# Kernel optimization log

Hardware: AMD Instinct MI355X
Metric: run time of the kernel (lower is better)

The kernel has to match this reference:

```python
import jax, jax.numpy as jnp
import numpy as np

IN_F, OUT_F, GROUP = 4096, 11008, 128
N_GROUPS = IN_F // GROUP  # 32 (in_features divisible by group_size -> no padding)


def setup_inputs() -> dict:
    key = jax.random.key(0)
    kx, kw, ks, kb = jax.random.split(key, 4)
    x = jax.random.normal(kx, (4, 2048, IN_F), dtype=jnp.float32)
    weight_q = jax.random.randint(kw, (OUT_F, IN_F), -128, 128, dtype=jnp.int32).astype(jnp.int8)
    scales = jax.random.uniform(ks, (OUT_F, N_GROUPS), dtype=jnp.float32) * 0.01 + 1e-4
    bias = jax.random.normal(kb, (OUT_F,), dtype=jnp.float32)
    return {"x": x, "weight_q": weight_q, "scales": scales, "bias": bias}


def reference(x, weight_q, scales, bias):
    # Dequantize: group-wise scale along in_features, cast to fp16 (as torch .half())
    W = (weight_q.astype(jnp.float32).reshape(OUT_F, N_GROUPS, GROUP)
         * scales[:, :, None]).reshape(OUT_F, IN_F).astype(jnp.float16)
    # fp16 linear: y = x W^T + b, then back to fp32
    y = jnp.einsum('bsi,oi->bso', x.astype(jnp.float16), W) + bias.astype(jnp.float16)
    return y.astype(jnp.float32)
```

## Files before the change

### kernel.cpp

```cpp
#include <hip/hip_runtime.h>

#define IN_F 4096
#define OUT_F 11008
#define NGROUPS 32
#define M_TOTAL 8192
#define BM 256
#define BN 256
#define BK 64
#define NKT (IN_F / BK)

typedef _Float16 half_t;
typedef __attribute__((ext_vector_type(8))) _Float16 half8;
typedef __attribute__((ext_vector_type(4))) _Float16 half4v;
typedef __attribute__((ext_vector_type(4))) float f32x4;
typedef __attribute__((ext_vector_type(4))) int i32x4;

typedef __attribute__((address_space(1))) const void gvoid_t;
typedef __attribute__((address_space(3))) void lvoid_t;

__global__ void convert_x_k(const float* __restrict__ x, half_t* __restrict__ xh) {
  const int n4 = M_TOTAL * IN_F / 4;
  int stride = gridDim.x * blockDim.x;
  for (int i = blockIdx.x * blockDim.x + threadIdx.x; i < n4; i += stride) {
    f32x4 v = __builtin_nontemporal_load((const f32x4*)x + i);
    half4v h;
    h[0] = (_Float16)v[0]; h[1] = (_Float16)v[1];
    h[2] = (_Float16)v[2]; h[3] = (_Float16)v[3];
    ((half4v*)xh)[i] = h;
  }
}

__global__ void dequant_w_k(const int* __restrict__ wq,
                            const float* __restrict__ scales,
                            half_t* __restrict__ wh) {
  int row = blockIdx.x;
  int t = threadIdx.x;
  size_t base = (size_t)row * IN_F + (size_t)t * 8;
  float s = scales[row * NGROUPS + (t >> 4)];
  i32x4 q0 = __builtin_nontemporal_load((const i32x4*)(wq + base));
  i32x4 q1 = __builtin_nontemporal_load((const i32x4*)(wq + base) + 1);
  half8 h;
#pragma unroll
  for (int j = 0; j < 4; ++j) h[j] = (_Float16)((float)q0[j] * s);
#pragma unroll
  for (int j = 0; j < 4; ++j) h[4 + j] = (_Float16)((float)q1[j] * s);
  *(half8*)(wh + base) = h;
}


__device__ __forceinline__ void rd4(half8 (&d)[4], const char* base) {
#pragma unroll
  for (int i = 0; i < 4; ++i) d[i] = *(const half8*)(base + i * 1024);
}

__device__ __forceinline__ void mfma16(f32x4 (&acc)[8][4], const half8 (&a)[4],
                                       const half8 (&b)[4], int mh) {
#pragma unroll
  for (int i = 0; i < 4; ++i)
#pragma unroll
    for (int j = 0; j < 4; ++j)
      acc[mh * 4 + i][j] =
          __builtin_amdgcn_mfma_f32_16x16x32_f16(a[i], b[j], acc[mh * 4 + i][j], 0, 0, 0);
}

#define BAR() __builtin_amdgcn_s_barrier()
#define SB0() __builtin_amdgcn_sched_barrier(0)
#define PRIO1() __builtin_amdgcn_s_setprio(1)
#define PRIO0() __builtin_amdgcn_s_setprio(0)
#define VMCNT(N) asm volatile("s_waitcnt vmcnt(" #N ")" ::: "memory")
#define LGKM(N) asm volatile("s_waitcnt lgkmcnt(" #N ")" ::: "memory")

#define STAGE(OP, KH, KT, S)                                                          \
  do {                                                                                \
    const half_t* g_ = ((OP) ? pBsrc : pAsrc) + (KT) * 64 + (KH) * 32;                \
    char* d_ = (char*)&lds[S][OP][KH][0] + wvoff;                                     \
    __builtin_amdgcn_global_load_lds((gvoid_t*)g_, (lvoid_t*)d_, 16, 0, 0);           \
    __builtin_amdgcn_global_load_lds((gvoid_t*)(g_ + 128 * IN_F),                     \
                                     (lvoid_t*)(d_ + 8192), 16, 0, 0);                \
  } while (0)

#define MPH(SL, KH, S1OP, S1KT, S1SL, S1KH, S2OP, S2KT, S2SL, S2KH, FENCE)   \
  do {                                                                       \
    rd4(a0, (const char*)&lds[SL][0][KH][0] + aoff);                         \
    rd4(a1, (const char*)&lds[SL][0][KH][0] + aoff + 4096);                  \
    rd4(b, (const char*)&lds[SL][1][KH][0] + boff);                          \
    STAGE(S1OP, S1KH, S1KT, S1SL);                                           \
    STAGE(S2OP, S2KH, S2KT, S2SL);                                           \
    SB0(); BAR();                                                            \
    LGKM(0); SB0(); PRIO1();                                                 \
    mfma16(acc, a0, b, 0);                                                   \
    mfma16(acc, a1, b, 1);                                                   \
    PRIO0();                                                                 \
    if ((FENCE) == 8) VMCNT(8);                                              \
    BAR(); SB0();                                                            \
  } while (0)

#define MPHN(SL, KH, FENCE)                                                  \
  do {                                                                       \
    rd4(a0, (const char*)&lds[SL][0][KH][0] + aoff);                         \
    rd4(a1, (const char*)&lds[SL][0][KH][0] + aoff + 4096);                  \
    rd4(b, (const char*)&lds[SL][1][KH][0] + boff);                          \
    SB0(); BAR();                                                            \
    LGKM(0); SB0(); PRIO1();                                                 \
    mfma16(acc, a0, b, 0);                                                   \
    mfma16(acc, a1, b, 1);                                                   \
    PRIO0();                                                                 \
    if ((FENCE) == 4) VMCNT(4);                                              \
    if ((FENCE) == 0) VMCNT(0);                                              \
    BAR(); SB0();                                                            \
  } while (0)

__global__ __launch_bounds__(512, 1) void gemm_k(const half_t* __restrict__ A,
                                                 const half_t* __restrict__ B,
                                                 const float* __restrict__ bias,
                                                 float* __restrict__ C) {
  __shared__ __align__(16) half_t lds[2][2][2][8192];

  const int tid = threadIdx.x;
  const int lane = tid & 63;
  const int wv = tid >> 6;
  const int wm = wv >> 2;
  const int wn = wv & 3;
  const int wvoff = wv << 10;

  const int nwg = gridDim.x;
  const int perx = nwg >> 3;
  const int L = ((int)blockIdx.x & 7) * perx + ((int)blockIdx.x >> 3);
  const int band = L >> 7;
  const int rr_ = L & 127;
  const int bn0 = band << 2;
  const int cols = (43 - bn0) < 4 ? (43 - bn0) : 4;
  const int bm = rr_ / cols;
  const int bn = bn0 + rr_ % cols;
  const int row0 = bm * BM;
  const int col0 = bn * BN;

  const int c16 = (tid & 3) * 16;
  const int srow = tid >> 2;
  const int clog = c16 ^ ((srow & 6) << 3);
  const int kidx = clog >> 1;
  const half_t* pAsrc = A + (size_t)(row0 + srow) * IN_F + kidx;
  const half_t* pBsrc = B + (size_t)(col0 + srow) * IN_F + kidx;

  const int r16 = lane & 15;
  const int kg = lane >> 4;
  const int arow = wm * 128 + r16;
  const int brow = wn * 64 + r16;
  const int aoff = arow * 64 + ((kg * 16) ^ ((arow & 6) << 3));
  const int boff = brow * 64 + ((kg * 16) ^ ((brow & 6) << 3));

  f32x4 acc[8][4];
#pragma unroll
  for (int m = 0; m < 8; ++m)
#pragma unroll
    for (int n = 0; n < 4; ++n) acc[m][n] = (f32x4){0.f, 0.f, 0.f, 0.f};

  STAGE(0, 0, 0, 0);
  STAGE(1, 0, 0, 0);
  STAGE(0, 1, 0, 0);
  STAGE(1, 1, 0, 0);
  STAGE(0, 0, 1, 1);
  STAGE(1, 0, 1, 1);
  VMCNT(4);
  BAR();
  SB0();

  half8 a0[4], a1[4], b[4];
  for (int u = 0; u < 31; ++u) {
    const int t1 = 2 * u + 1, n0 = 2 * u + 2, n1 = 2 * u + 3;
    MPH(0, 0, 0, t1, 1, 1, 1, t1, 1, 1, 8);
    MPH(0, 1, 0, n0, 0, 0, 1, n0, 0, 0, 8);
    MPH(1, 0, 0, n0, 0, 1, 1, n0, 0, 1, 8);
    MPH(1, 1, 0, n1, 1, 0, 1, n1, 1, 0, 8);
  }
  {
    MPH(0, 0, 0, 63, 1, 1, 1, 63, 1, 1, 8);
    MPHN(0, 1, 4);
    MPHN(1, 0, 0);
    MPHN(1, 1, -1);
  }

  const int kg4 = kg * 4;
#pragma unroll
  for (int nf = 0; nf < 4; ++nf) {
    int col = col0 + wn * 64 + nf * 16 + r16;
    _Float16 bh = (_Float16)bias[col];
#pragma unroll
    for (int mf = 0; mf < 8; ++mf) {
      int rb = row0 + wm * 128 + mf * 16 + kg4;
#pragma unroll
      for (int r = 0; r < 4; ++r) {
        _Float16 v = (_Float16)acc[mf][nf][r] + bh;
        __builtin_nontemporal_store((float)v, &C[(size_t)(rb + r) * OUT_F + col]);
      }
    }
  }
}

__global__ void naive_k(const float* __restrict__ x, const int* __restrict__ wq,
                        const float* __restrict__ scales, const float* __restrict__ bias,
                        float* __restrict__ out) {
  long idx = (long)blockIdx.x * blockDim.x + threadIdx.x;
  if (idx >= (long)M_TOTAL * OUT_F) return;
  int m = (int)(idx / OUT_F);
  int n = (int)(idx % OUT_F);
  float acc = 0.f;
  for (int g = 0; g < NGROUPS; ++g) {
    float s = scales[n * NGROUPS + g];
    for (int k = g * 128; k < (g + 1) * 128; ++k) {
      _Float16 xv = (_Float16)x[(size_t)m * IN_F + k];
      _Float16 wv = (_Float16)((float)wq[(size_t)n * IN_F + k] * s);
      acc += (float)xv * (float)wv;
    }
  }
  _Float16 r = (_Float16)acc + (_Float16)bias[n];
  out[idx] = (float)r;
}

extern "C" void kernel_launch(void* const* d_in, const int* in_sizes, int n_in,
                              void* d_out, int out_size, void* d_ws, size_t ws_size,
                              hipStream_t stream) {
  const float* x = (const float*)d_in[0];
  const int* wq = (const int*)d_in[1];
  const float* scales = (const float*)d_in[2];
  const float* bias = (const float*)d_in[3];
  float* out = (float*)d_out;

  const size_t xh_bytes = (size_t)M_TOTAL * IN_F * sizeof(half_t);
  const size_t wh_bytes = (size_t)OUT_F * IN_F * sizeof(half_t);

  if (ws_size >= xh_bytes + wh_bytes) {
    half_t* xh = (half_t*)d_ws;
    half_t* wh = (half_t*)((char*)d_ws + xh_bytes);
    convert_x_k<<<2048, 256, 0, stream>>>(x, xh);
    dequant_w_k<<<OUT_F, 512, 0, stream>>>(wq, scales, wh);
    gemm_k<<<(M_TOTAL / BM) * (OUT_F / BN), 512, 0, stream>>>(xh, wh, bias, out);
  } else {
    long total = (long)M_TOTAL * OUT_F;
    naive_k<<<(int)((total + 255) / 256), 256, 0, stream>>>(x, wq, scales, bias, out);
  }
}
```

Before: 786.8 us.

## Shrink GEMM tile to 256x128x32 with triple-buffered LDS and higher occupancy

Replaces the 256x256x64 tile, which used a double-buffered half-K pipeline at one block per CU, with a 256x128 tile and BK=32. LDS becomes three stages, prefetching two K-tiles ahead. Launch bounds now allow four blocks per CU, and the grid swizzle becomes a simple column-band mapping. Each wave holds a 64x64 accumulator instead of 128x64. The aim is more resident waves to hide latency, but each tile reuses its operands less, synchronises more often per FLOP, and needs a different grid size on the host.

```diff
diff --git a/kernel.cpp b/kernel.cpp
--- a/kernel.cpp
+++ b/kernel.cpp
@@ -5,8 +5,8 @@
 #define NGROUPS 32
 #define M_TOTAL 8192
 #define BM 256
-#define BN 256
-#define BK 64
+#define BN 128
+#define BK 32
 #define NKT (IN_F / BK)
 
 typedef _Float16 half_t;
@@ -48,21 +48,6 @@
 }
 
 
-__device__ __forceinline__ void rd4(half8 (&d)[4], const char* base) {
-#pragma unroll
-  for (int i = 0; i < 4; ++i) d[i] = *(const half8*)(base + i * 1024);
-}
-
-__device__ __forceinline__ void mfma16(f32x4 (&acc)[8][4], const half8 (&a)[4],
-                                       const half8 (&b)[4], int mh) {
-#pragma unroll
-  for (int i = 0; i < 4; ++i)
-#pragma unroll
-    for (int j = 0; j < 4; ++j)
-      acc[mh * 4 + i][j] =
-          __builtin_amdgcn_mfma_f32_16x16x32_f16(a[i], b[j], acc[mh * 4 + i][j], 0, 0, 0);
-}
-
 #define BAR() __builtin_amdgcn_s_barrier()
 #define SB0() __builtin_amdgcn_sched_barrier(0)
 #define PRIO1() __builtin_amdgcn_s_setprio(1)
@@ -70,70 +55,58 @@
 #define VMCNT(N) asm volatile("s_waitcnt vmcnt(" #N ")" ::: "memory")
 #define LGKM(N) asm volatile("s_waitcnt lgkmcnt(" #N ")" ::: "memory")
 
-#define STAGE(OP, KH, KT, S)                                                          \
-  do {                                                                                \
-    const half_t* g_ = ((OP) ? pBsrc : pAsrc) + (KT) * 64 + (KH) * 32;                \
-    char* d_ = (char*)&lds[S][OP][KH][0] + wvoff;                                     \
-    __builtin_amdgcn_global_load_lds((gvoid_t*)g_, (lvoid_t*)d_, 16, 0, 0);           \
-    __builtin_amdgcn_global_load_lds((gvoid_t*)(g_ + 128 * IN_F),                     \
-                                     (lvoid_t*)(d_ + 8192), 16, 0, 0);                \
+#define STAGE(KT, S)                                                                   \
+  do {                                                                                 \
+    char* sb_ = (char*)lds + (S) * 24576;                                              \
+    const half_t* gA_ = pAsrc + (KT) * 32;                                             \
+    const half_t* gB_ = pBsrc + (KT) * 32;                                             \
+    __builtin_amdgcn_global_load_lds((gvoid_t*)gA_, (lvoid_t*)(sb_ + t16), 16, 0, 0);  \
+    __builtin_amdgcn_global_load_lds((gvoid_t*)(gA_ + 128 * IN_F),                     \
+                                     (lvoid_t*)(sb_ + 8192 + t16), 16, 0, 0);          \
+    __builtin_amdgcn_global_load_lds((gvoid_t*)gB_,                                    \
+                                     (lvoid_t*)(sb_ + 16384 + t16), 16, 0, 0);         \
   } while (0)
 
-#define MPH(SL, KH, S1OP, S1KT, S1SL, S1KH, S2OP, S2KT, S2SL, S2KH, FENCE)   \
-  do {                                                                       \
-    rd4(a0, (const char*)&lds[SL][0][KH][0] + aoff);                         \
-    rd4(a1, (const char*)&lds[SL][0][KH][0] + aoff + 4096);                  \
-    rd4(b, (const char*)&lds[SL][1][KH][0] + boff);                          \
-    STAGE(S1OP, S1KH, S1KT, S1SL);                                           \
-    STAGE(S2OP, S2KH, S2KT, S2SL);                                           \
-    SB0(); BAR();                                                            \
-    LGKM(0); SB0(); PRIO1();                                                 \
-    mfma16(acc, a0, b, 0);                                                   \
-    mfma16(acc, a1, b, 1);                                                   \
-    PRIO0();                                                                 \
-    if ((FENCE) == 8) VMCNT(8);                                              \
-    BAR(); SB0();                                                            \
+#define RDPH(S)                                                         \
+  do {                                                                  \
+    const char* Ab_ = (const char*)lds + (S) * 24576;                   \
+    const char* Bb_ = Ab_ + 16384;                                      \
+    _Pragma("unroll") for (int m = 0; m < 4; ++m)                       \
+        a[m] = *(const half8*)(Ab_ + aoff + m * 1024);                  \
+    _Pragma("unroll") for (int n = 0; n < 4; ++n)                       \
+        b[n] = *(const half8*)(Bb_ + boff + n * 1024);                  \
   } while (0)
 
-#define MPHN(SL, KH, FENCE)                                                  \
-  do {                                                                       \
-    rd4(a0, (const char*)&lds[SL][0][KH][0] + aoff);                         \
-    rd4(a1, (const char*)&lds[SL][0][KH][0] + aoff + 4096);                  \
-    rd4(b, (const char*)&lds[SL][1][KH][0] + boff);                          \
-    SB0(); BAR();                                                            \
-    LGKM(0); SB0(); PRIO1();                                                 \
-    mfma16(acc, a0, b, 0);                                                   \
-    mfma16(acc, a1, b, 1);                                                   \
-    PRIO0();                                                                 \
-    if ((FENCE) == 4) VMCNT(4);                                              \
-    if ((FENCE) == 0) VMCNT(0);                                              \
-    BAR(); SB0();                                                            \
+#define DOMFMA()                                                        \
+  do {                                                                  \
+    _Pragma("unroll") for (int m = 0; m < 4; ++m)                       \
+        _Pragma("unroll") for (int n = 0; n < 4; ++n)                   \
+            acc[m][n] = __builtin_amdgcn_mfma_f32_16x16x32_f16(         \
+                a[m], b[n], acc[m][n], 0, 0, 0);                        \
   } while (0)
 
-__global__ __launch_bounds__(512, 1) void gemm_k(const half_t* __restrict__ A,
+__global__ __launch_bounds__(512, 4) void gemm_k(const half_t* __restrict__ A,
                                                  const half_t* __restrict__ B,
                                                  const float* __restrict__ bias,
                                                  float* __restrict__ C) {
-  __shared__ __align__(16) half_t lds[2][2][2][8192];
+  __shared__ __align__(16) char lds[3 * 24576];
 
   const int tid = threadIdx.x;
   const int lane = tid & 63;
   const int wv = tid >> 6;
-  const int wm = wv >> 2;
-  const int wn = wv & 3;
-  const int wvoff = wv << 10;
-
-  const int nwg = gridDim.x;
-  const int perx = nwg >> 3;
-  const int L = ((int)blockIdx.x & 7) * perx + ((int)blockIdx.x >> 3);
-  const int band = L >> 7;
-  const int rr_ = L & 127;
-  const int bn0 = band << 2;
-  const int cols = (43 - bn0) < 4 ? (43 - bn0) : 4;
-  const int bm = rr_ / cols;
-  const int bn = bn0 + rr_ % cols;
+  const int wr = wv & 3;
+  const int wc = wv >> 2;
+  const int t16 = tid * 16;
+
+  const int L = (int)blockIdx.x;
+  const int c_ = (L >> 8) < 10 ? (L >> 8) : 10;
+  const int r_ = L - (c_ << 8);
+  const int w_ = (c_ == 10) ? 6 : 8;
+  const int bm = (c_ == 10) ? (r_ / 6) : (r_ >> 3);
+  const int bn = c_ * 8 + ((c_ == 10) ? (r_ % 6) : (r_ & 7));
   const int row0 = bm * BM;
   const int col0 = bn * BN;
+  (void)w_;
 
   const int c16 = (tid & 3) * 16;
   const int srow = tid >> 2;
@@ -144,50 +117,58 @@
 
   const int r16 = lane & 15;
   const int kg = lane >> 4;
-  const int arow = wm * 128 + r16;
-  const int brow = wn * 64 + r16;
+  const int arow = wr * 64 + r16;
+  const int brow = wc * 64 + r16;
   const int aoff = arow * 64 + ((kg * 16) ^ ((arow & 6) << 3));
   const int boff = brow * 64 + ((kg * 16) ^ ((brow & 6) << 3));
 
-  f32x4 acc[8][4];
-#pragma unroll
-  for (int m = 0; m < 8; ++m)
+  f32x4 acc[4][4];
+#pragma unroll
+  for (int m = 0; m < 4; ++m)
 #pragma unroll
     for (int n = 0; n < 4; ++n) acc[m][n] = (f32x4){0.f, 0.f, 0.f, 0.f};
-
-  STAGE(0, 0, 0, 0);
-  STAGE(1, 0, 0, 0);
-  STAGE(0, 1, 0, 0);
-  STAGE(1, 1, 0, 0);
-  STAGE(0, 0, 1, 1);
-  STAGE(1, 0, 1, 1);
-  VMCNT(4);
+  half8 a[4], b[4];
+
+  STAGE(0, 0);
+  STAGE(1, 1);
+  VMCNT(3);
   BAR();
   SB0();
 
-  half8 a0[4], a1[4], b[4];
-  for (int u = 0; u < 31; ++u) {
-    const int t1 = 2 * u + 1, n0 = 2 * u + 2, n1 = 2 * u + 3;
-    MPH(0, 0, 0, t1, 1, 1, 1, t1, 1, 1, 8);
-    MPH(0, 1, 0, n0, 0, 0, 1, n0, 0, 0, 8);
-    MPH(1, 0, 0, n0, 0, 1, 1, n0, 0, 1, 8);
-    MPH(1, 1, 0, n1, 1, 0, 1, n1, 1, 0, 8);
+  for (int t = 0; t < NKT - 2; ++t) {
+    const int s = t % 3, s2 = (t + 2) % 3;
+    RDPH(s);
+    STAGE(t + 2, s2);
+    SB0(); BAR();
+    LGKM(0); SB0(); PRIO1();
+    DOMFMA();
+    PRIO0();
+    VMCNT(3);
+    BAR(); SB0();
   }
   {
-    MPH(0, 0, 0, 63, 1, 1, 1, 63, 1, 1, 8);
-    MPHN(0, 1, 4);
-    MPHN(1, 0, 0);
-    MPHN(1, 1, -1);
+    RDPH(0);
+    SB0(); BAR();
+    LGKM(0); SB0(); PRIO1();
+    DOMFMA();
+    PRIO0();
+    VMCNT(0);
+    BAR(); SB0();
+  }
+  {
+    RDPH(1);
+    LGKM(0); SB0();
+    DOMFMA();
   }
 
   const int kg4 = kg * 4;
 #pragma unroll
   for (int nf = 0; nf < 4; ++nf) {
-    int col = col0 + wn * 64 + nf * 16 + r16;
+    int col = col0 + wc * 64 + nf * 16 + r16;
     _Float16 bh = (_Float16)bias[col];
 #pragma unroll
-    for (int mf = 0; mf < 8; ++mf) {
-      int rb = row0 + wm * 128 + mf * 16 + kg4;
+    for (int mf = 0; mf < 4; ++mf) {
+      int rb = row0 + wr * 64 + mf * 16 + kg4;
 #pragma unroll
       for (int r = 0; r < 4; ++r) {
         _Float16 v = (_Float16)acc[mf][nf][r] + bh;
```

New measurement: 1.042 ms. 1.32x slower.
